# Performance work log

Measured on AMD Instinct MI355X. Metric: run time of the kernel, lower is better.

## Reference

```python
import jax, jax.numpy as jnp
import numpy as np
from jax import lax

TEMP = 0.05
MOMENTUM = 0.9
EPS = 1e-12


def _l2_normalize(x, axis=-1):
    n = jnp.sqrt(jnp.sum(x * x, axis=axis, keepdims=True))
    return x / jnp.maximum(n, EPS)


def _cross_entropy(logits, targets):
    # mean over batch of -log_softmax(logits)[target]
    logp = jax.nn.log_softmax(logits, axis=-1)
    return -jnp.mean(jnp.take_along_axis(logp, targets[:, None], axis=-1))


def _momentum_update(features, x, targets, m):
    # Sequential per-sample read-modify-write (faithful to the torch loop,
    # matters when targets contain duplicates). carry = memory bank.
    def step(f, xy):
        x_i, y_i = xy
        row = m * f[y_i] + (1.0 - m) * x_i
        row = row / jnp.linalg.norm(row)
        return f.at[y_i].set(row), None
    f, _ = lax.scan(step, features, (x, targets))
    return f


def setup_inputs() -> dict:
    key = jax.random.key(0)
    k1, k2, k3, k4, k5, k6 = jax.random.split(key, 6)
    B, D, N = 512, 1024, 16384
    inputs_rgb = jax.random.normal(k1, (B, D), dtype=jnp.float32)
    inputs_ir = jax.random.normal(k2, (B, D), dtype=jnp.float32)
    targets_rgb = jax.random.randint(k3, (B,), 0, N, dtype=jnp.int32)
    targets_ir = jax.random.randint(k4, (B,), 0, N, dtype=jnp.int32)
    # memory banks (buffers); initialized as normalized random rows to mimic a
    # warmed-up cluster memory (the module starts at zeros, degenerate for CE)
    features_rgb = _l2_normalize(jax.random.normal(k5, (N, D), dtype=jnp.float32))
    features_ir = _l2_normalize(jax.random.normal(k6, (N, D), dtype=jnp.float32))
    return {"inputs_rgb": inputs_rgb, "inputs_ir": inputs_ir,
            "targets_rgb": targets_rgb, "targets_ir": targets_ir,
            "features_rgb": features_rgb, "features_ir": features_ir}


def reference(inputs_rgb, inputs_ir, targets_rgb, targets_ir, features_rgb, features_ir):
    x_rgb = _l2_normalize(inputs_rgb)  # [B, D]
    x_ir = _l2_normalize(inputs_ir)
    logits_rgb = (x_rgb @ features_rgb.T) / TEMP  # [B, N]
    logits_ir = (x_ir @ features_ir.T) / TEMP
    loss_rgb = _cross_entropy(logits_rgb, targets_rgb)
    loss_ir = _cross_entropy(logits_ir, targets_ir)
    # side-effect of CM.backward in the original: momentum scatter update + renorm
    # (change_scale == 1.0 so the Hungarian cross-modal exchange is skipped)
    new_features_rgb = _momentum_update(features_rgb, x_rgb, targets_rgb, MOMENTUM)
    new_features_ir = _momentum_update(features_ir, x_ir, targets_ir, MOMENTUM)
    return (loss_rgb, loss_ir, new_features_rgb, new_features_ir)
```

## Files before the change

kernel.cpp:

```cpp
#include <hip/hip_runtime.h>
#include <math.h>

#define BATCH 512
#define DIM   1024
#define NCLUS 16384
#define TINV  20.0f

typedef __attribute__((ext_vector_type(4))) float f32x4;
typedef __attribute__((ext_vector_type(8))) short bf16x8;

static __device__ __forceinline__ unsigned short f2bf(float f) {
  unsigned int u = __float_as_uint(f);
  u += 0x7FFFu + ((u >> 16) & 1u);
  return (unsigned short)(u >> 16);
}

typedef const __attribute__((address_space(1))) unsigned int* gas1_t;
typedef __attribute__((address_space(3))) unsigned int* las3_t;
static __device__ __forceinline__ void gload16(const void* g, void* l) {
  __builtin_amdgcn_global_load_lds((gas1_t)g, (las3_t)l, 16, 0, 0);
}

__global__ void nrm_kernel(const float* __restrict__ in_rgb,
                           const float* __restrict__ in_ir,
                           float* __restrict__ xf,
                           unsigned short* __restrict__ xb,
                           float* __restrict__ accum) {
  int gid = blockIdx.x * blockDim.x + threadIdx.x;
  if (gid < 2048) accum[gid] = 0.0f;

  int row = blockIdx.x;
  int mod = row >> 9;
  int r   = row & 511;
  const float* in = (mod ? in_ir : in_rgb) + (size_t)r * DIM;
  float* xo          = xf + ((size_t)mod * BATCH + r) * DIM;
  unsigned short* xbo = xb + ((size_t)mod * BATCH + r) * DIM;

  int t = threadIdx.x;
  float4 v = ((const float4*)in)[t];
  float ss = v.x*v.x + v.y*v.y + v.z*v.z + v.w*v.w;
#pragma unroll
  for (int m = 1; m < 64; m <<= 1) ss += __shfl_xor(ss, m, 64);
  __shared__ float red[4];
  if ((t & 63) == 0) red[t >> 6] = ss;
  __syncthreads();
  float inv = 1.0f / fmaxf(sqrtf(red[0] + red[1] + red[2] + red[3]), 1e-12f);
  float4 o = make_float4(v.x * inv, v.y * inv, v.z * inv, v.w * inv);
  ((float4*)xo)[t] = o;
  ushort4 ob = make_ushort4(f2bf(o.x), f2bf(o.y), f2bf(o.z), f2bf(o.w));
  ((ushort4*)xbo)[t] = ob;
}

#define BM 128
#define BN 128
#define BK 32
#define NSTEP (DIM / BK)

__global__ void gemm_lse_kernel(const unsigned short* __restrict__ xb,
                                const float* __restrict__ f_rgb,
                                const float* __restrict__ f_ir,
                                const int* __restrict__ t_rgb,
                                const int* __restrict__ t_ir,
                                float* __restrict__ outc,
                                float* __restrict__ rowsum,
                                float* __restrict__ tgtlog) {
  const int nt  = blockIdx.x;
  const int bt  = blockIdx.y & 3;
  const int mod = blockIdx.y >> 2;

  const unsigned short* X = xb + ((size_t)mod * BATCH + bt * BM) * DIM;
  const float* Ff = (mod ? f_ir : f_rgb) + (size_t)nt * BN * DIM;
  float* Oc = outc + ((size_t)mod * NCLUS + (size_t)nt * BN) * DIM;
  const int*   tg = mod ? t_ir : t_rgb;
  float* rs = rowsum + mod * BATCH;
  float* tl = tgtlog + mod * BATCH;

  __shared__ __align__(16) unsigned short As[2][BM * BK];
  __shared__ __align__(16) unsigned short Bs[2][BN * BK];

  const int tid  = threadIdx.x;
  const int wid  = tid >> 6;
  const int lane = tid & 63;
  const int wr = wid >> 1, wc = wid & 1;
  const int l15 = lane & 15, lhi = lane >> 4;

  f32x4 acc[4][4];
#pragma unroll
  for (int m = 0; m < 4; ++m)
#pragma unroll
    for (int n = 0; n < 4; ++n) acc[m][n] = (f32x4){0.f, 0.f, 0.f, 0.f};

  auto B_LOAD = [&](float4* br, int kk) {
#pragma unroll
    for (int i = 0; i < 4; ++i) {
      int id = i * 256 + tid;
      br[i] = *(const float4*)(Ff + (size_t)(id >> 3) * DIM + kk + ((id & 7) << 2));
    }
  };
  auto B_WRITE = [&](int buf, const float4* br, int kk) {
#pragma unroll
    for (int i = 0; i < 4; ++i) {
      int id = i * 256 + tid;
      int row = id >> 3, c4 = (id & 7) << 2;
      float4 v = br[i];
      *(ushort4*)(&Bs[buf][row * BK + c4]) =
          make_ushort4(f2bf(v.x), f2bf(v.y), f2bf(v.z), f2bf(v.w));
      if (bt == 0) {
        float2* o2 = (float2*)(Oc + (size_t)row * DIM + kk + c4);
        o2[0] = make_float2(v.x, v.y);
        o2[1] = make_float2(v.z, v.w);
      }
    }
  };
  auto A_STAGE = [&](int buf, int kk) {
#pragma unroll
    for (int i = 0; i < 2; ++i) {
      int q = i * 256 + tid;
      gload16(X + (size_t)(q >> 2) * DIM + kk + (q & 3) * 8,
              &As[buf][(size_t)(i * 256 + wid * 64) * 8]);
    }
  };

  auto COMPUTE = [&](int buf) {
    bf16x8 a[4], b[4];
#pragma unroll
    for (int m = 0; m < 4; ++m)
      a[m] = *(const bf16x8*)(&As[buf][(wr * 64 + m * 16 + l15) * BK + lhi * 8]);
#pragma unroll
    for (int n = 0; n < 4; ++n)
      b[n] = *(const bf16x8*)(&Bs[buf][(wc * 64 + n * 16 + l15) * BK + lhi * 8]);
#pragma unroll
    for (int m = 0; m < 4; ++m)
#pragma unroll
      for (int n = 0; n < 4; ++n)
        acc[m][n] = __builtin_amdgcn_mfma_f32_16x16x32_bf16(a[m], b[n], acc[m][n], 0, 0, 0);
  };

  {
    float4 br[4];
    B_LOAD(br, 0);
    A_STAGE(0, 0);
    B_WRITE(0, br, 0);
  }
  __syncthreads();
  int cur = 0;
  for (int s = 1; s < NSTEP; ++s) {
    float4 brn[4];
    B_LOAD(brn, s * BK);
    COMPUTE(cur);
    A_STAGE(cur ^ 1, s * BK);
    B_WRITE(cur ^ 1, brn, s * BK);
    __syncthreads();
    cur ^= 1;
  }
  COMPUTE(cur);

#pragma unroll
  for (int m = 0; m < 4; ++m) {
    const int browbase = bt * BM + wr * 64 + m * 16 + lhi * 4;
    float esum[4];
#pragma unroll
    for (int j = 0; j < 4; ++j) {
      const int brow = browbase + j;
      const int t = tg[brow];
      float e = 0.f;
#pragma unroll
      for (int n = 0; n < 4; ++n) {
        float logit = acc[m][n][j] * TINV;
        e += __expf(logit);
        int col = nt * BN + wc * 64 + n * 16 + l15;
        if (col == t) tl[brow] = logit;
      }
      esum[j] = e;
    }
#pragma unroll
    for (int j = 0; j < 4; ++j) {
      float e = esum[j];
      e += __shfl_xor(e, 1, 64);
      e += __shfl_xor(e, 2, 64);
      e += __shfl_xor(e, 4, 64);
      e += __shfl_xor(e, 8, 64);
      if (l15 == 0) atomicAdd(rs + browbase + j, e);
    }
  }
}

__global__ void loss_kernel(const float* __restrict__ rowsum,
                            const float* __restrict__ tgtlog,
                            float* __restrict__ out) {
  int t = threadIdx.x;
  float lr = logf(rowsum[t]) - tgtlog[t];
  float li = logf(rowsum[BATCH + t]) - tgtlog[BATCH + t];
#pragma unroll
  for (int m = 1; m < 64; m <<= 1) { lr += __shfl_xor(lr, m, 64); li += __shfl_xor(li, m, 64); }
  __shared__ float sr[8], si[8];
  if ((t & 63) == 0) { sr[t >> 6] = lr; si[t >> 6] = li; }
  __syncthreads();
  if (t == 0) {
    float a = 0.f, b = 0.f;
#pragma unroll
    for (int i = 0; i < 8; ++i) { a += sr[i]; b += si[i]; }
    out[0] = a * (1.0f / BATCH);
    out[1] = b * (1.0f / BATCH);
  }
}

__global__ void mom_kernel(const int* __restrict__ t_rgb,
                           const int* __restrict__ t_ir,
                           const float* __restrict__ xf,
                           float* __restrict__ out) {
  const int i   = blockIdx.x;
  const int mod = blockIdx.y;
  const int* tg = mod ? t_ir : t_rgb;
  const int y = tg[i];
  for (int j = 0; j < i; ++j)
    if (tg[j] == y) return;

  const float* x = xf + (size_t)mod * BATCH * DIM;
  float* rowp = out + (size_t)mod * NCLUS * DIM + (size_t)y * DIM;

  const int t = threadIdx.x;
  float2 r0 = ((const float2*)rowp)[t];
  float2 r1 = ((const float2*)rowp)[t + 256];
  __shared__ float red[4];

  for (int j = i; j < BATCH; ++j) {
    if (tg[j] != y) continue;
    const float2* xr = (const float2*)(x + (size_t)j * DIM);
    float2 x0 = xr[t], x1 = xr[t + 256];
    r0.x = 0.9f * r0.x + 0.1f * x0.x;
    r0.y = 0.9f * r0.y + 0.1f * x0.y;
    r1.x = 0.9f * r1.x + 0.1f * x1.x;
    r1.y = 0.9f * r1.y + 0.1f * x1.y;
    float ss = r0.x*r0.x + r0.y*r0.y + r1.x*r1.x + r1.y*r1.y;
#pragma unroll
    for (int m = 1; m < 64; m <<= 1) ss += __shfl_xor(ss, m, 64);
    if ((t & 63) == 0) red[t >> 6] = ss;
    __syncthreads();
    float tot = red[0] + red[1] + red[2] + red[3];
    __syncthreads();
    float inv = 1.0f / sqrtf(tot);
    r0.x *= inv; r0.y *= inv; r1.x *= inv; r1.y *= inv;
  }
  ((float2*)rowp)[t] = r0;
  ((float2*)rowp)[t + 256] = r1;
}

extern "C" void kernel_launch(void* const* d_in, const int* in_sizes, int n_in,
                              void* d_out, int out_size, void* d_ws, size_t ws_size,
                              hipStream_t stream) {
  (void)in_sizes; (void)n_in; (void)out_size; (void)ws_size;
  const float* in_rgb = (const float*)d_in[0];
  const float* in_ir  = (const float*)d_in[1];
  const int*   t_rgb  = (const int*)d_in[2];
  const int*   t_ir   = (const int*)d_in[3];
  const float* f_rgb  = (const float*)d_in[4];
  const float* f_ir   = (const float*)d_in[5];
  float* out = (float*)d_out;

  char* ws = (char*)d_ws;
  float*          xf     = (float*)ws;
  unsigned short* xb     = (unsigned short*)(ws + (4u<<20));
  float*          rowsum = (float*)(ws + (6u<<20));
  float*          tgtlog = rowsum + 1024;

  nrm_kernel<<<1024, 256, 0, stream>>>(in_rgb, in_ir, xf, xb, rowsum);
  gemm_lse_kernel<<<dim3(128, 8), 256, 0, stream>>>(xb, f_rgb, f_ir, t_rgb, t_ir,
                                                    out + 2, rowsum, tgtlog);
  mom_kernel<<<dim3(512, 2), 256, 0, stream>>>(t_rgb, t_ir, xf, out + 2);
  loss_kernel<<<1, 512, 0, stream>>>(rowsum, tgtlog, out);
}
```

Measured before the change: 195.5 us.

## Split memory-bank copy into separate blocks; load B operand directly into registers

The GEMM+LSE kernel becomes a fused launch. Odd block slots do a nontemporal streaming copy of both feature banks into the output, and even slots do the GEMM, so the copy no longer sits inside the bt==0 GEMM blocks. The B operand is loaded from global memory straight into registers and packed to bf16 by truncation, skipping the LDS round-trip and the rounding step. The change also adds an XOR swizzle on the A tile in LDS, XCD-aware block-to-tile mapping for L2 reuse, launch bounds, and a manual waitcnt/barrier schedule. In exchange, the feature banks are now read a second time by the copy blocks, and truncating to bf16 slightly changes numerics.

```diff
diff --git a/kernel.cpp b/kernel.cpp
--- a/kernel.cpp
+++ b/kernel.cpp
@@ -7,6 +7,7 @@
 #define TINV  20.0f
 
 typedef __attribute__((ext_vector_type(4))) float f32x4;
+typedef __attribute__((ext_vector_type(2))) float f32x2;
 typedef __attribute__((ext_vector_type(8))) short bf16x8;
 
 static __device__ __forceinline__ unsigned short f2bf(float f) {
@@ -52,37 +53,56 @@
 }
 
 #define BM 128
-#define BN 128
 #define BK 32
 #define NSTEP (DIM / BK)
 
-__global__ void gemm_lse_kernel(const unsigned short* __restrict__ xb,
-                                const float* __restrict__ f_rgb,
-                                const float* __restrict__ f_ir,
-                                const int* __restrict__ t_rgb,
-                                const int* __restrict__ t_ir,
-                                float* __restrict__ outc,
-                                float* __restrict__ rowsum,
-                                float* __restrict__ tgtlog) {
-  const int nt  = blockIdx.x;
-  const int bt  = blockIdx.y & 3;
-  const int mod = blockIdx.y >> 2;
+__launch_bounds__(256, 2)
+__global__ void fused_kernel(const unsigned short* __restrict__ xb,
+                             const float* __restrict__ f_rgb,
+                             const float* __restrict__ f_ir,
+                             const int* __restrict__ t_rgb,
+                             const int* __restrict__ t_ir,
+                             float* __restrict__ outc,
+                             float* __restrict__ rowsum,
+                             float* __restrict__ tgtlog) {
+  const int xcd = blockIdx.x & 7;
+  const int o   = blockIdx.x >> 3;
+  const int tid = threadIdx.x;
+
+  if (o & 1) {
+    const size_t n4 = (size_t)NCLUS * DIM / 4;
+    const int cid = (o >> 1) * 8 + xcd;
+    for (size_t i = (size_t)cid * 256 + tid; i < 2 * n4; i += 1024 * 256) {
+      const f32x4* src = (i < n4) ? ((const f32x4*)f_rgb) + i
+                                  : ((const f32x4*)f_ir) + (i - n4);
+      const f32x4 v = __builtin_nontemporal_load(src);
+      f32x2* o2 = (f32x2*)(outc + 4 * i);
+      __builtin_nontemporal_store((f32x2){v.x, v.y}, o2);
+      __builtin_nontemporal_store((f32x2){v.z, v.w}, o2 + 1);
+    }
+    return;
+  }
+
+  const int j   = o >> 1;
+  const int nt  = xcd + 8 * (j >> 3);
+  const int bt  = j & 3;
+  const int mod = (j >> 2) & 1;
 
   const unsigned short* X = xb + ((size_t)mod * BATCH + bt * BM) * DIM;
-  const float* Ff = (mod ? f_ir : f_rgb) + (size_t)nt * BN * DIM;
-  float* Oc = outc + ((size_t)mod * NCLUS + (size_t)nt * BN) * DIM;
-  const int*   tg = mod ? t_ir : t_rgb;
+  const float* Fbase = mod ? f_ir : f_rgb;
+  const int* tg = mod ? t_ir : t_rgb;
   float* rs = rowsum + mod * BATCH;
   float* tl = tgtlog + mod * BATCH;
 
   __shared__ __align__(16) unsigned short As[2][BM * BK];
-  __shared__ __align__(16) unsigned short Bs[2][BN * BK];
-
-  const int tid  = threadIdx.x;
+
   const int wid  = tid >> 6;
   const int lane = tid & 63;
   const int wr = wid >> 1, wc = wid & 1;
   const int l15 = lane & 15, lhi = lane >> 4;
+  const int sw = (l15 & 6) << 3;
+
+  const float* Fp = Fbase + ((size_t)nt * BM + wc * 64 + l15) * DIM + lhi * 8;
 
   f32x4 acc[4][4];
 #pragma unroll
@@ -90,97 +110,93 @@
 #pragma unroll
     for (int n = 0; n < 4; ++n) acc[m][n] = (f32x4){0.f, 0.f, 0.f, 0.f};
 
-  auto B_LOAD = [&](float4* br, int kk) {
-#pragma unroll
-    for (int i = 0; i < 4; ++i) {
-      int id = i * 256 + tid;
-      br[i] = *(const float4*)(Ff + (size_t)(id >> 3) * DIM + kk + ((id & 7) << 2));
-    }
-  };
-  auto B_WRITE = [&](int buf, const float4* br, int kk) {
-#pragma unroll
-    for (int i = 0; i < 4; ++i) {
-      int id = i * 256 + tid;
-      int row = id >> 3, c4 = (id & 7) << 2;
-      float4 v = br[i];
-      *(ushort4*)(&Bs[buf][row * BK + c4]) =
-          make_ushort4(f2bf(v.x), f2bf(v.y), f2bf(v.z), f2bf(v.w));
-      if (bt == 0) {
-        float2* o2 = (float2*)(Oc + (size_t)row * DIM + kk + c4);
-        o2[0] = make_float2(v.x, v.y);
-        o2[1] = make_float2(v.z, v.w);
-      }
-    }
-  };
-  auto A_STAGE = [&](int buf, int kk) {
-#pragma unroll
-    for (int i = 0; i < 2; ++i) {
-      int q = i * 256 + tid;
-      gload16(X + (size_t)(q >> 2) * DIM + kk + (q & 3) * 8,
-              &As[buf][(size_t)(i * 256 + wid * 64) * 8]);
-    }
-  };
-
-  auto COMPUTE = [&](int buf) {
-    bf16x8 a[4], b[4];
+  auto STAGE_A = [&](int buf, int kt) {
+#pragma unroll
+    for (int c = 0; c < 2; ++c) {
+      int q = c * 256 + tid;
+      int cs = (q & 3) ^ ((q >> 3) & 3);
+      gload16(X + (size_t)(q >> 2) * DIM + kt * BK + cs * 8,
+              &As[buf][(c * 256 + wid * 64) * 8]);
+    }
+  };
+  auto B_LOAD = [&](f32x4* raw, int kk) {
+#pragma unroll
+    for (int n = 0; n < 4; ++n) {
+      raw[2 * n]     = *(const f32x4*)(Fp + (size_t)n * 16 * DIM + kk);
+      raw[2 * n + 1] = *(const f32x4*)(Fp + (size_t)n * 16 * DIM + kk + 4);
+    }
+  };
+  auto PACK = [&](const f32x4* raw, bf16x8* pk) {
+#pragma unroll
+    for (int n = 0; n < 4; ++n) {
+      union { bf16x8 v; unsigned int u[4]; } t;
+      const unsigned int* a0 = (const unsigned int*)&raw[2 * n];
+      const unsigned int* a1 = (const unsigned int*)&raw[2 * n + 1];
+      t.u[0] = (a0[0] >> 16) | (a0[1] & 0xFFFF0000u);
+      t.u[1] = (a0[2] >> 16) | (a0[3] & 0xFFFF0000u);
+      t.u[2] = (a1[0] >> 16) | (a1[1] & 0xFFFF0000u);
+      t.u[3] = (a1[2] >> 16) | (a1[3] & 0xFFFF0000u);
+      pk[n] = t.v;
+    }
+  };
+  auto LDA = [&](int buf, int row) {
+    return *(const bf16x8*)((const char*)As[buf] + ((row * 64 + lhi * 16) ^ sw));
+  };
+  auto COMPUTE = [&](int buf, const bf16x8* pk) {
+    bf16x8 a[4];
+#pragma unroll
+    for (int m = 0; m < 4; ++m) a[m] = LDA(buf, wr * 64 + m * 16 + l15);
 #pragma unroll
     for (int m = 0; m < 4; ++m)
-      a[m] = *(const bf16x8*)(&As[buf][(wr * 64 + m * 16 + l15) * BK + lhi * 8]);
-#pragma unroll
-    for (int n = 0; n < 4; ++n)
-      b[n] = *(const bf16x8*)(&Bs[buf][(wc * 64 + n * 16 + l15) * BK + lhi * 8]);
-#pragma unroll
-    for (int m = 0; m < 4; ++m)
 #pragma unroll
       for (int n = 0; n < 4; ++n)
-        acc[m][n] = __builtin_amdgcn_mfma_f32_16x16x32_bf16(a[m], b[n], acc[m][n], 0, 0, 0);
-  };
-
-  {
-    float4 br[4];
-    B_LOAD(br, 0);
-    A_STAGE(0, 0);
-    B_WRITE(0, br, 0);
-  }
+        acc[m][n] = __builtin_amdgcn_mfma_f32_16x16x32_bf16(a[m], pk[n], acc[m][n], 0, 0, 0);
+  };
+
+  f32x4 raw[8];
+  bf16x8 pk[4];
+  B_LOAD(raw, 0);
+  STAGE_A(0, 0);
   __syncthreads();
-  int cur = 0;
-  for (int s = 1; s < NSTEP; ++s) {
-    float4 brn[4];
-    B_LOAD(brn, s * BK);
-    COMPUTE(cur);
-    A_STAGE(cur ^ 1, s * BK);
-    B_WRITE(cur ^ 1, brn, s * BK);
-    __syncthreads();
-    cur ^= 1;
-  }
-  COMPUTE(cur);
+
+  for (int s = 0; s < NSTEP - 1; ++s) {
+    PACK(raw, pk);
+    STAGE_A((s + 1) & 1, s + 1);
+    B_LOAD(raw, (s + 1) * BK);
+    COMPUTE(s & 1, pk);
+    asm volatile("s_waitcnt vmcnt(8) lgkmcnt(0)" ::: "memory");
+    __builtin_amdgcn_sched_barrier(0);
+    __builtin_amdgcn_s_barrier();
+  }
+  PACK(raw, pk);
+  COMPUTE((NSTEP - 1) & 1, pk);
 
 #pragma unroll
   for (int m = 0; m < 4; ++m) {
     const int browbase = bt * BM + wr * 64 + m * 16 + lhi * 4;
     float esum[4];
 #pragma unroll
-    for (int j = 0; j < 4; ++j) {
-      const int brow = browbase + j;
+    for (int j2 = 0; j2 < 4; ++j2) {
+      const int brow = browbase + j2;
       const int t = tg[brow];
       float e = 0.f;
 #pragma unroll
       for (int n = 0; n < 4; ++n) {
-        float logit = acc[m][n][j] * TINV;
+        float logit = acc[m][n][j2] * TINV;
         e += __expf(logit);
-        int col = nt * BN + wc * 64 + n * 16 + l15;
+        int col = nt * BM + wc * 64 + n * 16 + l15;
         if (col == t) tl[brow] = logit;
       }
-      esum[j] = e;
-    }
-#pragma unroll
-    for (int j = 0; j < 4; ++j) {
-      float e = esum[j];
+      esum[j2] = e;
+    }
+#pragma unroll
+    for (int j2 = 0; j2 < 4; ++j2) {
+      float e = esum[j2];
       e += __shfl_xor(e, 1, 64);
       e += __shfl_xor(e, 2, 64);
       e += __shfl_xor(e, 4, 64);
       e += __shfl_xor(e, 8, 64);
-      if (l15 == 0) atomicAdd(rs + browbase + j, e);
+      if (l15 == 0) atomicAdd(rs + browbase + j2, e);
     }
   }
 }
@@ -265,8 +281,8 @@
   float*          tgtlog = rowsum + 1024;
 
   nrm_kernel<<<1024, 256, 0, stream>>>(in_rgb, in_ir, xf, xb, rowsum);
-  gemm_lse_kernel<<<dim3(128, 8), 256, 0, stream>>>(xb, f_rgb, f_ir, t_rgb, t_ir,
-                                                    out + 2, rowsum, tgtlog);
+  fused_kernel<<<2048, 256, 0, stream>>>(xb, f_rgb, f_ir, t_rgb, t_ir,
+                                         out + 2, rowsum, tgtlog);
   mom_kernel<<<dim3(512, 2), 256, 0, stream>>>(t_rgb, t_ir, xf, out + 2);
   loss_kernel<<<1, 512, 0, stream>>>(rowsum, tgtlog, out);
 }
```

Result: slower. 335.6 us (+71.6%).

## Swizzle LDS tiles, split feature-bank copy across row tiles, restructure prefetch pipeline

Applied to the files above, without the earlier changes.

Applies an XOR swizzle to the A and B shared-memory tiles to reduce bank conflicts on the MFMA fragment reads. The fp32-to-bf16 conversion of B switches from round-to-nearest to plain truncation. The copy of the feature bank into the output, previously done only by bt==0 blocks, is now spread across all four batch-tile blocks with nontemporal stores. The loop issues next-stage loads before compute and uses explicit waitcnt, barriers and launch bounds. Truncation changes numerics slightly, and the hand-written waitcnt counts risk subtle races.

```diff
diff --git a/kernel.cpp b/kernel.cpp
--- a/kernel.cpp
+++ b/kernel.cpp
@@ -7,6 +7,7 @@
 #define TINV  20.0f
 
 typedef __attribute__((ext_vector_type(4))) float f32x4;
+typedef __attribute__((ext_vector_type(2))) float f32x2;
 typedef __attribute__((ext_vector_type(8))) short bf16x8;
 
 static __device__ __forceinline__ unsigned short f2bf(float f) {
@@ -54,8 +55,9 @@
 #define BM 128
 #define BN 128
 #define BK 32
-#define NSTEP (DIM / BK)
-
+#define KT_N (DIM / BK)
+
+__launch_bounds__(256, 4)
 __global__ void gemm_lse_kernel(const unsigned short* __restrict__ xb,
                                 const float* __restrict__ f_rgb,
                                 const float* __restrict__ f_ir,
@@ -70,8 +72,9 @@
 
   const unsigned short* X = xb + ((size_t)mod * BATCH + bt * BM) * DIM;
   const float* Ff = (mod ? f_ir : f_rgb) + (size_t)nt * BN * DIM;
-  float* Oc = outc + ((size_t)mod * NCLUS + (size_t)nt * BN) * DIM;
-  const int*   tg = mod ? t_ir : t_rgb;
+  const float* Fq = Ff + (size_t)bt * 32 * DIM;
+  float* Oq = outc + ((size_t)mod * NCLUS + (size_t)nt * BN + bt * 32) * DIM;
+  const int* tg = mod ? t_ir : t_rgb;
   float* rs = rowsum + mod * BATCH;
   float* tl = tgtlog + mod * BATCH;
 
@@ -83,6 +86,7 @@
   const int lane = tid & 63;
   const int wr = wid >> 1, wc = wid & 1;
   const int l15 = lane & 15, lhi = lane >> 4;
+  const int sw = (l15 & 6) << 3;
 
   f32x4 acc[4][4];
 #pragma unroll
@@ -90,45 +94,50 @@
 #pragma unroll
     for (int n = 0; n < 4; ++n) acc[m][n] = (f32x4){0.f, 0.f, 0.f, 0.f};
 
-  auto B_LOAD = [&](float4* br, int kk) {
-#pragma unroll
-    for (int i = 0; i < 4; ++i) {
-      int id = i * 256 + tid;
-      br[i] = *(const float4*)(Ff + (size_t)(id >> 3) * DIM + kk + ((id & 7) << 2));
-    }
-  };
-  auto B_WRITE = [&](int buf, const float4* br, int kk) {
-#pragma unroll
-    for (int i = 0; i < 4; ++i) {
-      int id = i * 256 + tid;
-      int row = id >> 3, c4 = (id & 7) << 2;
-      float4 v = br[i];
-      *(ushort4*)(&Bs[buf][row * BK + c4]) =
-          make_ushort4(f2bf(v.x), f2bf(v.y), f2bf(v.z), f2bf(v.w));
-      if (bt == 0) {
-        float2* o2 = (float2*)(Oc + (size_t)row * DIM + kk + c4);
-        o2[0] = make_float2(v.x, v.y);
-        o2[1] = make_float2(v.z, v.w);
-      }
-    }
-  };
-  auto A_STAGE = [&](int buf, int kk) {
-#pragma unroll
-    for (int i = 0; i < 2; ++i) {
-      int q = i * 256 + tid;
-      gload16(X + (size_t)(q >> 2) * DIM + kk + (q & 3) * 8,
-              &As[buf][(size_t)(i * 256 + wid * 64) * 8]);
-    }
-  };
-
+  auto A_STAGE = [&](int buf, int kt) {
+#pragma unroll
+    for (int c = 0; c < 2; ++c) {
+      int q = c * 256 + tid;
+      int cs = (q & 3) ^ ((q >> 3) & 3);
+      gload16(X + (size_t)(q >> 2) * DIM + kt * BK + cs * 8,
+              &As[buf][(c * 256 + wid * 64) * 8]);
+    }
+  };
+  auto B_LOAD = [&](f32x4* br, int kk) {
+#pragma unroll
+    for (int c = 0; c < 2; ++c) {
+      int h = c * 256 + tid, row = h >> 2, j = h & 3;
+      const float* sp = Ff + (size_t)row * DIM + kk + j * 8;
+      br[c * 2]     = *(const f32x4*)sp;
+      br[c * 2 + 1] = *(const f32x4*)(sp + 4);
+    }
+  };
+  auto B_WRITE = [&](int buf, const f32x4* br) {
+#pragma unroll
+    for (int c = 0; c < 2; ++c) {
+      int h = c * 256 + tid, row = h >> 2, j = h & 3;
+      union { bf16x8 v; unsigned int w[4]; } p;
+      const unsigned int* x0 = (const unsigned int*)&br[c * 2];
+      const unsigned int* x1 = (const unsigned int*)&br[c * 2 + 1];
+      p.w[0] = (x0[0] >> 16) | (x0[1] & 0xFFFF0000u);
+      p.w[1] = (x0[2] >> 16) | (x0[3] & 0xFFFF0000u);
+      p.w[2] = (x1[0] >> 16) | (x1[1] & 0xFFFF0000u);
+      p.w[3] = (x1[2] >> 16) | (x1[3] & 0xFFFF0000u);
+      *(bf16x8*)((char*)&Bs[buf][0] + row * 64 + ((j ^ ((row >> 1) & 3)) << 4)) = p.v;
+    }
+  };
+  auto LDA = [&](int buf, int row) {
+    return *(const bf16x8*)((const char*)As[buf] + ((row * 64 + lhi * 16) ^ sw));
+  };
+  auto LDB = [&](int buf, int row) {
+    return *(const bf16x8*)((const char*)Bs[buf] + ((row * 64 + lhi * 16) ^ sw));
+  };
   auto COMPUTE = [&](int buf) {
     bf16x8 a[4], b[4];
 #pragma unroll
-    for (int m = 0; m < 4; ++m)
-      a[m] = *(const bf16x8*)(&As[buf][(wr * 64 + m * 16 + l15) * BK + lhi * 8]);
-#pragma unroll
-    for (int n = 0; n < 4; ++n)
-      b[n] = *(const bf16x8*)(&Bs[buf][(wc * 64 + n * 16 + l15) * BK + lhi * 8]);
+    for (int n = 0; n < 4; ++n) b[n] = LDB(buf, wc * 64 + n * 16 + l15);
+#pragma unroll
+    for (int m = 0; m < 4; ++m) a[m] = LDA(buf, wr * 64 + m * 16 + l15);
 #pragma unroll
     for (int m = 0; m < 4; ++m)
 #pragma unroll
@@ -137,23 +146,37 @@
   };
 
   {
-    float4 br[4];
-    B_LOAD(br, 0);
+    f32x4 br0[4];
+    B_LOAD(br0, 0);
     A_STAGE(0, 0);
-    B_WRITE(0, br, 0);
+    B_WRITE(0, br0);
   }
   __syncthreads();
-  int cur = 0;
-  for (int s = 1; s < NSTEP; ++s) {
-    float4 brn[4];
-    B_LOAD(brn, s * BK);
+
+  for (int s = 0; s < KT_N; ++s) {
+    const int cur = s & 1;
+    const int id = s * 256 + tid;
+    const int r32 = id >> 8, col = id & 255;
+    f32x4 craw = *((const f32x4*)(Fq + (size_t)r32 * DIM) + col);
+    f32x4 braw[4];
+    if (s + 1 < KT_N) {
+      B_LOAD(braw, (s + 1) * BK);
+      A_STAGE(cur ^ 1, s + 1);
+    }
+    __builtin_amdgcn_sched_barrier(0);
     COMPUTE(cur);
-    A_STAGE(cur ^ 1, s * BK);
-    B_WRITE(cur ^ 1, brn, s * BK);
-    __syncthreads();
-    cur ^= 1;
-  }
-  COMPUTE(cur);
+    if (s + 1 < KT_N) B_WRITE(cur ^ 1, braw);
+    {
+      float* dp = Oq + (size_t)r32 * DIM + (size_t)col * 4;
+      __builtin_nontemporal_store((f32x2){craw.x, craw.y}, (f32x2*)dp);
+      __builtin_nontemporal_store((f32x2){craw.z, craw.w}, (f32x2*)(dp + 2));
+    }
+    if (s + 1 < KT_N) {
+      asm volatile("s_waitcnt vmcnt(2) lgkmcnt(0)" ::: "memory");
+      __builtin_amdgcn_sched_barrier(0);
+      __builtin_amdgcn_s_barrier();
+    }
+  }
 
 #pragma unroll
   for (int m = 0; m < 4; ++m) {
```

New measurement: 170.1 us, median of 3. 13.0% less time.
